# Performance work log

Hardware: AMD Instinct MI355X
Metric: run time of the kernel (lower is better)

Reference implementation:

```python
import jax, jax.numpy as jnp
import numpy as np

N = 4096
E = 262144
IN_C = 128
OUT_C = 128
EDGE_D = 16


def setup_inputs() -> dict:
    key = jax.random.key(0)
    k = jax.random.split(key, 8)
    x = jax.random.normal(k[0], (N, IN_C), dtype=jnp.float32)
    edge_index = jax.random.randint(k[1], (2, E), 0, N, dtype=jnp.int64)
    edge_attr = jax.random.normal(k[2], (N, N, EDGE_D), dtype=jnp.float32)
    # nn.Linear params: y = x @ W.T + b; store pre-transposed W for x @ W
    s1 = 1.0 / np.sqrt(IN_C + EDGE_D)
    s2 = 1.0 / np.sqrt(OUT_C)
    W1 = jax.random.uniform(k[3], (IN_C + EDGE_D, OUT_C), jnp.float32, -s1, s1)
    b1 = jax.random.uniform(k[4], (OUT_C,), jnp.float32, -s1, s1)
    W2 = jax.random.uniform(k[5], (OUT_C, OUT_C), jnp.float32, -s2, s2)
    b2 = jax.random.uniform(k[6], (OUT_C,), jnp.float32, -s2, s2)
    return {"x": x, "edge_index": edge_index, "edge_attr": edge_attr,
            "W1": W1, "b1": b1, "W2": W2, "b2": b2}


def reference(x, edge_index, edge_attr, W1, b1, W2, b2):
    row, col = edge_index[0], edge_index[1]
    x_row = x[row]                      # [E, IN_C] gather
    e = edge_attr[row, col]             # [E, EDGE_D] gather from dense NxN table
    h = jnp.concatenate([x_row, e], axis=-1)     # [E, IN_C+EDGE_D]
    h = jax.nn.relu(h @ W1 + b1)                  # [E, OUT_C]
    h = jax.nn.relu(h @ W2 + b2)                  # [E, OUT_C]
    # global_add_pool(out, col): scatter-add edges into node buckets by col
    return jax.ops.segment_sum(h, col, num_segments=x.shape[0])  # [N, OUT_C]
```

## Files before the change

kernel.cpp:

```cpp
#include <hip/hip_runtime.h>
#include <hip/hip_bf16.h>

#define NN 4096
#define IC 128
#define OC 128
#define ED 16
#define EPB 64
#define NT 256
#define NSLOT 8
#define NBLK 512
#define NCPY 8

typedef __bf16 bf16x8 __attribute__((ext_vector_type(8)));
typedef float  f32x16 __attribute__((ext_vector_type(16)));

#define BAR() do { asm volatile("s_waitcnt lgkmcnt(0)" ::: "memory"); \
    __builtin_amdgcn_s_barrier(); \
    __builtin_amdgcn_sched_barrier(0); } while (0)

__device__ __forceinline__ unsigned short bf16u(float f) {
    unsigned int u = __float_as_uint(f);
    u = (u + 0x7FFFu + ((u >> 16) & 1u)) >> 16;
    return (unsigned short)u;
}
__device__ __forceinline__ float bf16tof(unsigned short h) {
    return __uint_as_float(((unsigned int)h) << 16);
}
__device__ __forceinline__ int swzk(int row) { return (row ^ (row >> 3)) & 7; }

__global__ __launch_bounds__(128) void k_xw1(
    const float* __restrict__ x, const float* __restrict__ W1,
    const float* __restrict__ b1, const int* __restrict__ eidx,
    float* __restrict__ xw1b, float* __restrict__ out,
    int* __restrict__ hist8, int E)
{
    __shared__ float xs[8][IC];
    const int t = threadIdx.x;
    const int r0 = blockIdx.x * 8;
    #pragma unroll
    for (int r = 0; r < 8; ++r) xs[r][t] = x[(size_t)(r0 + r) * IC + t];

    const float4 z = make_float4(0.f, 0.f, 0.f, 0.f);
    float4* o4 = (float4*)out;
    o4[blockIdx.x * 256 + t]       = z;
    o4[blockIdx.x * 256 + 128 + t] = z;

    {
        const int e0 = blockIdx.x * 512;
        #pragma unroll
        for (int j = 0; j < 4; ++j) {
            const int k = (2 * blockIdx.x + (j >> 1)) & (NCPY - 1);
            atomicAdd(&hist8[k * 4096 + eidx[E + e0 + t + j * 128]], 1);
        }
    }

    __syncthreads();
    float acc[8];
    const float bb = b1[t];
    #pragma unroll
    for (int r = 0; r < 8; ++r) acc[r] = bb;
    #pragma unroll 4
    for (int k = 0; k < IC; ++k) {
        const float w = W1[(size_t)k * OC + t];
        #pragma unroll
        for (int r = 0; r < 8; ++r) acc[r] = fmaf(xs[r][k], w, acc[r]);
    }
    #pragma unroll
    for (int r = 0; r < 8; ++r) xw1b[(size_t)(r0 + r) * OC + t] = acc[r];
}

__global__ __launch_bounds__(256) void k_scan(
    const int* __restrict__ hist8, int* __restrict__ cursor8)
{
    __shared__ int tot[256];
    __shared__ int base[256];
    const int t = threadIdx.x;
    int loc[16];
    int s = 0;
    #pragma unroll
    for (int j = 0; j < 16; ++j) {
        const int b = t * 16 + j;
        int sb = 0;
        #pragma unroll
        for (int k = 0; k < NCPY; ++k) sb += hist8[k * 4096 + b];
        loc[j] = s; s += sb;
    }
    tot[t] = s;
    __syncthreads();
    if (t == 0) {
        int a = 0;
        for (int i = 0; i < 256; ++i) { base[i] = a; a += tot[i]; }
    }
    __syncthreads();
    const int a = base[t];
    #pragma unroll
    for (int j = 0; j < 16; ++j) {
        const int b = t * 16 + j;
        int off = a + loc[j];
        #pragma unroll
        for (int k = 0; k < NCPY; ++k) {
            cursor8[k * 4096 + b] = off;
            off += hist8[k * 4096 + b];
        }
    }
}

__global__ void k_scatter(const int* __restrict__ eidx, int* __restrict__ cursor8,
                          int2* __restrict__ csr, int E) {
    const int i = blockIdx.x * blockDim.x + threadIdx.x;
    const int k = blockIdx.x & (NCPY - 1);
    if (i < E) {
        const int row = eidx[i];
        const int col = eidx[E + i];
        const int pos = atomicAdd(&cursor8[k * 4096 + col], 1);
        csr[pos] = make_int2(row, col);
    }
}

__global__ __launch_bounds__(NT, 2) void k_edge9(
    const int2* __restrict__ csr, const float* __restrict__ eattr,
    const float* __restrict__ xw1b, const float* __restrict__ W1,
    const float* __restrict__ W2, const float* __restrict__ b2,
    float* __restrict__ out, int E)
{
    extern __shared__ char smem[];
    char*   const h1hi = smem;
    char*   const h1lo = smem + 16384;
    float4* const eaL  = (float4*)(smem + 32768);
    float4* const w1L  = (float4*)(smem + 40960);
    float*  const lacc = (float*)(smem + 49152);
    int*    const srowL = (int*)(smem + 53248);
    int*    const scolL = srowL + 256;

    const int t   = threadIdx.x;
    const int l   = t & 63;
    const int wid = t >> 6;
    const int cg  = t & 15, eg = t >> 4;
    const int c0  = cg << 3, e0 = eg << 2;
    const int sz  = (eg >> 1) & 3;
    const int em  = t >> 2, q = t & 3;
    const int esz = (em >> 3) & 3;

    const int lm  = l & 31;
    const int hi  = l >> 5;
    const int c2  = wid * 32 + lm;

    w1L[t]       = ((const float4*)(W1 + (size_t)IC * OC))[t];
    w1L[t + NT]  = ((const float4*)(W1 + (size_t)IC * OC))[t + NT];

    bf16x8 w2h[8], w2l[8];
    #pragma unroll
    for (int s = 0; s < 8; ++s) {
        union { unsigned short us[8]; bf16x8 v; } Uh, Ul;
        #pragma unroll
        for (int j = 0; j < 8; ++j) {
            const float w = W2[(size_t)(s * 16 + hi * 8 + j) * OC + c2];
            const unsigned short h = bf16u(w);
            Uh.us[j] = h;
            Ul.us[j] = bf16u(w - bf16tof(h));
        }
        w2h[s] = Uh.v; w2l[s] = Ul.v;
    }
    const float b2s = b2[c2];

    #pragma unroll
    for (int i = 0; i < 4; ++i) lacc[t + NT * i] = 0.f;

    const int nper = (E / EPB) / NBLK;
    const int ibb  = blockIdx.x * nper;

    if (t < EPB) {
        const int2 r0v = csr[(size_t)ibb * EPB + t];
        srowL[t] = r0v.x; scolL[t] = r0v.y;
        const int ib1 = (nper > 1) ? 1 : 0;
        const int2 r1v = csr[(size_t)(ibb + ib1) * EPB + t];
        srowL[64 + t] = r1v.x; scolL[64 + t] = r1v.y;
    }
    __syncthreads();

    float4 pA;
    {
        const int r = srowL[em], c = scolL[em];
        pA = ((const float4*)(eattr + ((size_t)r * NN + c) * ED))[q];
    }
    eaL[(em * 4 + q) ^ esz] = pA;
    float4 xa[4], xb[4];
    #pragma unroll
    for (int ri = 0; ri < 4; ++ri) {
        const int row = srowL[e0 + ri];
        const float4* p = (const float4*)(xw1b + (size_t)row * OC + c0);
        xa[ri] = p[0]; xb[ri] = p[1];
    }
    int2 pidx;
    {
        const int ib2 = (nper > 2) ? 2 : (nper - 1);
        pidx = (t < EPB) ? csr[(size_t)(ibb + ib2) * EPB + t] : make_int2(0, 0);
    }
    __syncthreads();

    for (int ii = 0; ii < nper; ++ii) {
        const int cb  = ii & 1;
        const int ib4 = ii & 3;

        float4 ha[4], hb[4];
        #pragma unroll
        for (int ri = 0; ri < 4; ++ri) { ha[ri] = xa[ri]; hb[ri] = xb[ri]; }
        #pragma unroll
        for (int dc = 0; dc < 4; ++dc) {
            float4 ev[4];
            #pragma unroll
            for (int ri = 0; ri < 4; ++ri)
                ev[ri] = eaL[cb * 256 + ((((e0 + ri) * 4 + dc)) ^ sz)];
            #pragma unroll
            for (int dd = 0; dd < 4; ++dd) {
                const int d = dc * 4 + dd;
                const float4 wA = w1L[d * 32 + cg * 2];
                const float4 wB = w1L[d * 32 + cg * 2 + 1];
                #pragma unroll
                for (int ri = 0; ri < 4; ++ri) {
                    const float evd = (dd == 0) ? ev[ri].x : (dd == 1) ? ev[ri].y
                                     : (dd == 2) ? ev[ri].z : ev[ri].w;
                    ha[ri].x = fmaf(evd, wA.x, ha[ri].x);
                    ha[ri].y = fmaf(evd, wA.y, ha[ri].y);
                    ha[ri].z = fmaf(evd, wA.z, ha[ri].z);
                    ha[ri].w = fmaf(evd, wA.w, ha[ri].w);
                    hb[ri].x = fmaf(evd, wB.x, hb[ri].x);
                    hb[ri].y = fmaf(evd, wB.y, hb[ri].y);
                    hb[ri].z = fmaf(evd, wB.z, hb[ri].z);
                    hb[ri].w = fmaf(evd, wB.w, hb[ri].w);
                }
            }
        }
        #pragma unroll
        for (int ri = 0; ri < 4; ++ri) {
            const int row = e0 + ri;
            float v[8] = { ha[ri].x, ha[ri].y, ha[ri].z, ha[ri].w,
                           hb[ri].x, hb[ri].y, hb[ri].z, hb[ri].w };
            union { unsigned short us[8]; uint4 qv; } Hh, Hl;
            #pragma unroll
            for (int j = 0; j < 8; ++j) {
                const float f = fmaxf(v[j], 0.f);
                const unsigned short h = bf16u(f);
                Hh.us[j] = h;
                Hl.us[j] = bf16u(f - bf16tof(h));
            }
            const int boff = (cg * 16) ^ (swzk(row) << 4);
            *(uint4*)(h1hi + row * 256 + boff) = Hh.qv;
            *(uint4*)(h1lo + row * 256 + boff) = Hl.qv;
        }
        if (t < EPB) {
            srowL[((ii + 2) & 3) * 64 + t] = pidx.x;
            scolL[((ii + 2) & 3) * 64 + t] = pidx.y;
        }
        {
            const int jn = (ii + 1) & 3;
            const int r = srowL[jn * 64 + em], c = scolL[jn * 64 + em];
            pA = ((const float4*)(eattr + ((size_t)r * NN + c) * ED))[q];
            #pragma unroll
            for (int ri = 0; ri < 4; ++ri) {
                const int row = srowL[jn * 64 + e0 + ri];
                const float4* p = (const float4*)(xw1b + (size_t)row * OC + c0);
                xa[ri] = p[0]; xb[ri] = p[1];
            }
        }
        {
            const int iin = (ii + 3 < nper) ? (ii + 3) : (nper - 1);
            pidx = (t < EPB) ? csr[(size_t)(ibb + iin) * EPB + t] : make_int2(0, 0);
        }
        BAR();

        f32x16 acc0 = (f32x16)(0.0f);
        f32x16 acc1 = (f32x16)(0.0f);
        const int arow0 = lm;
        const int arow1 = 32 + lm;
        const int ak0 = swzk(arow0) << 4;
        const int ak1 = swzk(arow1) << 4;
        #pragma unroll
        for (int s = 0; s < 8; ++s) {
            const int kb = s * 32 + hi * 16;
            const bf16x8 aH0 = *(const bf16x8*)(h1hi + arow0 * 256 + (kb ^ ak0));
            const bf16x8 aL0 = *(const bf16x8*)(h1lo + arow0 * 256 + (kb ^ ak0));
            const bf16x8 aH1 = *(const bf16x8*)(h1hi + arow1 * 256 + (kb ^ ak1));
            const bf16x8 aL1 = *(const bf16x8*)(h1lo + arow1 * 256 + (kb ^ ak1));
            acc0 = __builtin_amdgcn_mfma_f32_32x32x16_bf16(aH0, w2h[s], acc0, 0, 0, 0);
            acc1 = __builtin_amdgcn_mfma_f32_32x32x16_bf16(aH1, w2h[s], acc1, 0, 0, 0);
            acc0 = __builtin_amdgcn_mfma_f32_32x32x16_bf16(aL0, w2h[s], acc0, 0, 0, 0);
            acc1 = __builtin_amdgcn_mfma_f32_32x32x16_bf16(aL1, w2h[s], acc1, 0, 0, 0);
            acc0 = __builtin_amdgcn_mfma_f32_32x32x16_bf16(aH0, w2l[s], acc0, 0, 0, 0);
            acc1 = __builtin_amdgcn_mfma_f32_32x32x16_bf16(aH1, w2l[s], acc1, 0, 0, 0);
        }

        const int colbase = scolL[ib4 * 64];
        #pragma unroll
        for (int p = 0; p < 2; ++p) {
            const int mbase = p * 32 + 4 * hi;
            #pragma unroll
            for (int g = 0; g < 4; ++g) {
                const int eb = mbase + 8 * g;
                float sv;
                {
                    const float a0 = (p == 0) ? acc0[4 * g] : acc1[4 * g];
                    sv = fmaxf(a0 + b2s, 0.f);
                }
                int ccur = scolL[ib4 * 64 + eb];
                #pragma unroll
                for (int j = 1; j < 4; ++j) {
                    const float aj = (p == 0) ? acc0[4 * g + j] : acc1[4 * g + j];
                    const float v = fmaxf(aj + b2s, 0.f);
                    const int c = scolL[ib4 * 64 + eb + j];
                    if (c == ccur) {
                        sv += v;
                    } else {
                        const int slot = ccur - colbase;
                        if (slot < NSLOT) {
                            if (sv != 0.f) atomicAdd(&lacc[slot * OC + c2], sv);
                        } else {
                            if (sv != 0.f) atomicAdd(&out[(size_t)ccur * OC + c2], sv);
                        }
                        ccur = c; sv = v;
                    }
                }
                const int slot = ccur - colbase;
                if (slot < NSLOT) {
                    if (sv != 0.f) atomicAdd(&lacc[slot * OC + c2], sv);
                } else {
                    if (sv != 0.f) atomicAdd(&out[(size_t)ccur * OC + c2], sv);
                }
            }
        }
        eaL[(cb ^ 1) * 256 + ((em * 4 + q) ^ esz)] = pA;
        BAR();

        int span = scolL[ib4 * 64 + EPB - 1] - colbase + 1;
        if (span > NSLOT) span = NSLOT;
        for (int idx = t; idx < span * OC; idx += NT) {
            const float v = lacc[idx];
            lacc[idx] = 0.f;
            if (v != 0.f)
                atomicAdd(&out[(size_t)(colbase + (idx >> 7)) * OC + (idx & 127)], v);
        }
    }
}

#define LDS_BYTES 55296

extern "C" void kernel_launch(void* const* d_in, const int* in_sizes, int n_in,
                              void* d_out, int out_size, void* d_ws, size_t ws_size,
                              hipStream_t stream) {
    const float* x    = (const float*)d_in[0];
    const int*   eidx = (const int*)d_in[1];
    const float* ea   = (const float*)d_in[2];
    const float* W1   = (const float*)d_in[3];
    const float* b1   = (const float*)d_in[4];
    const float* W2   = (const float*)d_in[5];
    const float* b2   = (const float*)d_in[6];
    float* out = (float*)d_out;

    const int E = in_sizes[1] / 2;

    char* ws = (char*)d_ws;
    float* xw1b    = (float*)ws;
    int*   hist8   = (int*)(ws + 2097152);
    int*   cursor8 = (int*)(ws + 2097152 + 131072);
    int2*  csr     = (int2*)(ws + 2097152 + 262144);

    hipMemsetAsync(hist8, 0, 131072, stream);
    k_xw1<<<NN / 8, 128, 0, stream>>>(x, W1, b1, eidx, xw1b, out, hist8, E);
    k_scan<<<1, 256, 0, stream>>>(hist8, cursor8);
    k_scatter<<<(E + 255) / 256, 256, 0, stream>>>(eidx, cursor8, csr, E);

    hipFuncSetAttribute(reinterpret_cast<const void*>(k_edge9),
                        hipFuncAttributeMaxDynamicSharedMemorySize, LDS_BYTES);
    k_edge9<<<NBLK, NT, LDS_BYTES, stream>>>(csr, ea, xw1b, W1, W2, b2, out, E);
}
```

Baseline: 139.1 us.

## Accumulate block-wide column buckets in LDS and flush once per block

Each block now keeps a 16-slot LDS accumulator anchored at its first column for its whole edge range, instead of flushing 8 slots to global memory after every 64-edge tile. At the end, the scan's column start offsets are used to decide whether the block owns a column completely. Owned columns get a plain store and shared columns get an atomic add. This removes the per-tile flush loop, its barriers and most global atomics, at the cost of slightly more LDS and a new colstart array. It relies on `out` having been zeroed earlier, since owned columns overwrite it, and on each block's edges spanning about 16 columns so few fall back to global atomics.

```diff
diff --git a/kernel.cpp b/kernel.cpp
--- a/kernel.cpp
+++ b/kernel.cpp
@@ -7,7 +7,7 @@
 #define ED 16
 #define EPB 64
 #define NT 256
-#define NSLOT 8
+#define NSLOT 16
 #define NBLK 512
 #define NCPY 8
 
@@ -70,7 +70,8 @@
 }
 
 __global__ __launch_bounds__(256) void k_scan(
-    const int* __restrict__ hist8, int* __restrict__ cursor8)
+    const int* __restrict__ hist8, int* __restrict__ cursor8,
+    int* __restrict__ colstart, int E)
 {
     __shared__ int tot[256];
     __shared__ int base[256];
@@ -97,12 +98,14 @@
     for (int j = 0; j < 16; ++j) {
         const int b = t * 16 + j;
         int off = a + loc[j];
+        colstart[b] = off;
         #pragma unroll
         for (int k = 0; k < NCPY; ++k) {
             cursor8[k * 4096 + b] = off;
             off += hist8[k * 4096 + b];
         }
     }
+    if (t == 0) colstart[4096] = E;
 }
 
 __global__ void k_scatter(const int* __restrict__ eidx, int* __restrict__ cursor8,
@@ -117,11 +120,11 @@
     }
 }
 
-__global__ __launch_bounds__(NT, 2) void k_edge9(
+__global__ __launch_bounds__(NT, 2) void k_edge10(
     const int2* __restrict__ csr, const float* __restrict__ eattr,
     const float* __restrict__ xw1b, const float* __restrict__ W1,
     const float* __restrict__ W2, const float* __restrict__ b2,
-    float* __restrict__ out, int E)
+    const int* __restrict__ colstart, float* __restrict__ out, int E)
 {
     extern __shared__ char smem[];
     char*   const h1hi = smem;
@@ -129,7 +132,7 @@
     float4* const eaL  = (float4*)(smem + 32768);
     float4* const w1L  = (float4*)(smem + 40960);
     float*  const lacc = (float*)(smem + 49152);
-    int*    const srowL = (int*)(smem + 53248);
+    int*    const srowL = (int*)(smem + 57344);
     int*    const scolL = srowL + 256;
 
     const int t   = threadIdx.x;
@@ -164,7 +167,7 @@
     const float b2s = b2[c2];
 
     #pragma unroll
-    for (int i = 0; i < 4; ++i) lacc[t + NT * i] = 0.f;
+    for (int i = 0; i < NSLOT * OC / NT; ++i) lacc[t + NT * i] = 0.f;
 
     const int nper = (E / EPB) / NBLK;
     const int ibb  = blockIdx.x * nper;
@@ -177,6 +180,7 @@
         srowL[64 + t] = r1v.x; scolL[64 + t] = r1v.y;
     }
     __syncthreads();
+    const int colbase0 = scolL[0];
 
     float4 pA;
     {
@@ -290,7 +294,6 @@
             acc1 = __builtin_amdgcn_mfma_f32_32x32x16_bf16(aH1, w2l[s], acc1, 0, 0, 0);
         }
 
-        const int colbase = scolL[ib4 * 64];
         #pragma unroll
         for (int p = 0; p < 2; ++p) {
             const int mbase = p * 32 + 4 * hi;
@@ -311,7 +314,7 @@
                     if (c == ccur) {
                         sv += v;
                     } else {
-                        const int slot = ccur - colbase;
+                        const int slot = ccur - colbase0;
                         if (slot < NSLOT) {
                             if (sv != 0.f) atomicAdd(&lacc[slot * OC + c2], sv);
                         } else {
@@ -320,7 +323,7 @@
                         ccur = c; sv = v;
                     }
                 }
-                const int slot = ccur - colbase;
+                const int slot = ccur - colbase0;
                 if (slot < NSLOT) {
                     if (sv != 0.f) atomicAdd(&lacc[slot * OC + c2], sv);
                 } else {
@@ -330,19 +333,29 @@
         }
         eaL[(cb ^ 1) * 256 + ((em * 4 + q) ^ esz)] = pA;
         BAR();
-
-        int span = scolL[ib4 * 64 + EPB - 1] - colbase + 1;
-        if (span > NSLOT) span = NSLOT;
-        for (int idx = t; idx < span * OC; idx += NT) {
-            const float v = lacc[idx];
-            lacc[idx] = 0.f;
-            if (v != 0.f)
-                atomicAdd(&out[(size_t)(colbase + (idx >> 7)) * OC + (idx & 127)], v);
-        }
-    }
-}
-
-#define LDS_BYTES 55296
+    }
+
+    const int blk_e0 = ibb * EPB;
+    const int blk_e1 = blk_e0 + nper * EPB;
+    #pragma unroll 1
+    for (int s = 0; s < NSLOT; ++s) {
+        const int c = colbase0 + s;
+        if (c >= NN) break;
+        const int cs = colstart[c];
+        const int ce = colstart[c + 1];
+        if (ce <= blk_e0 || cs >= blk_e1) continue;
+        if (t < OC) {
+            const float v = lacc[s * OC + t];
+            if (cs >= blk_e0 && ce <= blk_e1) {
+                out[(size_t)c * OC + t] = v;
+            } else if (v != 0.f) {
+                atomicAdd(&out[(size_t)c * OC + t], v);
+            }
+        }
+    }
+}
+
+#define LDS_BYTES 59392
 
 extern "C" void kernel_launch(void* const* d_in, const int* in_sizes, int n_in,
                               void* d_out, int out_size, void* d_ws, size_t ws_size,
@@ -359,17 +372,19 @@
     const int E = in_sizes[1] / 2;
 
     char* ws = (char*)d_ws;
-    float* xw1b    = (float*)ws;
-    int*   hist8   = (int*)(ws + 2097152);
-    int*   cursor8 = (int*)(ws + 2097152 + 131072);
-    int2*  csr     = (int2*)(ws + 2097152 + 262144);
+    float* xw1b     = (float*)ws;
+    int*   hist8    = (int*)(ws + 2097152);
+    int*   cursor8  = (int*)(ws + 2097152 + 131072);
+    int*   colstart = (int*)(ws + 2097152 + 262144);
+    int2*  csr      = (int2*)(ws + 2097152 + 294912);
 
     hipMemsetAsync(hist8, 0, 131072, stream);
     k_xw1<<<NN / 8, 128, 0, stream>>>(x, W1, b1, eidx, xw1b, out, hist8, E);
-    k_scan<<<1, 256, 0, stream>>>(hist8, cursor8);
+    k_scan<<<1, 256, 0, stream>>>(hist8, cursor8, colstart, E);
     k_scatter<<<(E + 255) / 256, 256, 0, stream>>>(eidx, cursor8, csr, E);
 
-    hipFuncSetAttribute(reinterpret_cast<const void*>(k_edge9),
+    hipFuncSetAttribute(reinterpret_cast<const void*>(k_edge10),
                         hipFuncAttributeMaxDynamicSharedMemorySize, LDS_BYTES);
-    k_edge9<<<NBLK, NT, LDS_BYTES, stream>>>(csr, ea, xw1b, W1, W2, b2, out, E);
-}
+    k_edge10<<<NBLK, NT, LDS_BYTES, stream>>>(csr, ea, xw1b, W1, W2, b2,
+                                              colstart, out, E);
+}
```

Measured after the change: 142.0 us. 2.0% more time.
